# Kernel optimization log

Measured on AMD Instinct MI355X. Metric: run time of the kernel, lower is better.

## Reference

```python
import jax, jax.numpy as jnp
import numpy as np

DIM = 1024
HEADS = 16
HEAD_DIM = DIM // HEADS
FF = 4 * DIM


def setup_inputs() -> dict:
    key = jax.random.key(0)
    ks = jax.random.split(key, 16)
    s = 0.02
    return {
        "x": jax.random.normal(ks[0], (2, 2048, DIM), dtype=jnp.float32),
        "wq": jax.random.normal(ks[1], (DIM, DIM), dtype=jnp.float32) * s,
        "bq": jnp.zeros((DIM,), jnp.float32),
        "wk": jax.random.normal(ks[2], (DIM, DIM), dtype=jnp.float32) * s,
        "bk": jnp.zeros((DIM,), jnp.float32),
        "wv": jax.random.normal(ks[3], (DIM, DIM), dtype=jnp.float32) * s,
        "bv": jnp.zeros((DIM,), jnp.float32),
        "wo": jax.random.normal(ks[4], (DIM, DIM), dtype=jnp.float32) * s,
        "bo": jnp.zeros((DIM,), jnp.float32),
        "w1": jax.random.normal(ks[5], (DIM, FF), dtype=jnp.float32) * s,
        "b1": jnp.zeros((FF,), jnp.float32),
        "w2": jax.random.normal(ks[6], (FF, DIM), dtype=jnp.float32) * s,
        "b2": jnp.zeros((DIM,), jnp.float32),
        "g1": jnp.ones((DIM,), jnp.float32),
        "be1": jnp.zeros((DIM,), jnp.float32),
        "g2": jnp.ones((DIM,), jnp.float32),
        "be2": jnp.zeros((DIM,), jnp.float32),
    }


def _layernorm(x, g, b, eps=1e-5):
    mu = jnp.mean(x, axis=-1, keepdims=True)
    var = jnp.mean(jnp.square(x - mu), axis=-1, keepdims=True)
    return (x - mu) * jax.lax.rsqrt(var + eps) * g + b


def reference(x, wq, bq, wk, bk, wv, bv, wo, bo, w1, b1, w2, b2, g1, be1, g2, be2):
    B, T, D = x.shape
    normed = _layernorm(x, g1, be1)
    # [B,T,D] -> [B,H,T,hd]
    def heads(y):
        return y.reshape(B, T, HEADS, HEAD_DIM).transpose(0, 2, 1, 3)
    q = heads(normed @ wq + bq)
    k = heads(normed @ wk + bk)
    v = heads(normed @ wv + bv)
    scale = 1.0 / np.sqrt(HEAD_DIM).astype(np.float32)
    attn = jax.nn.softmax(jnp.einsum('bhqd,bhkd->bhqk', q, k) * scale, axis=-1)
    out = jnp.einsum('bhqk,bhkd->bhqd', attn, v)
    out = out.transpose(0, 2, 1, 3).reshape(B, T, D)
    x = x + out @ wo + bo
    h = _layernorm(x, g2, be2)
    ffn = jax.nn.gelu(h @ w1 + b1, approximate=False) @ w2 + b2
    return x + ffn
```

## Files before the change

kernel.cpp:

```cpp
#include <hip/hip_runtime.h>
#include <math.h>

#define DIM   1024
#define HEADS 16
#define HDIM  64
#define FFDIM 4096
#define MROWS 4096
#define SEQ   2048
#define QKVS  3072
#define SCALE_Q 0.1803368801111204f

typedef _Float16 f16x8 __attribute__((ext_vector_type(8)));
typedef _Float16 f16x4 __attribute__((ext_vector_type(4)));
typedef float    f32x4 __attribute__((ext_vector_type(4)));

#define GLOAD_LDS16(g, l) __builtin_amdgcn_global_load_lds(                 \
    (const __attribute__((address_space(1))) void*)(g),                     \
    (__attribute__((address_space(3))) void*)(l), 16, 0, 0)

__device__ __forceinline__ float gelu_exact(float x) {
    return 0.5f * x * (1.0f + erff(x * 0.70710678118654752f));
}

__device__ __forceinline__ int pk2(float a, float b) {
    union { _Float16 h[2]; int i; } u;
    u.h[0] = (_Float16)a; u.h[1] = (_Float16)b;
    return u.i;
}

__global__ __launch_bounds__(256) void ln_kernel(
    const float* __restrict__ x, const float* __restrict__ g,
    const float* __restrict__ b, _Float16* __restrict__ out)
{
    const int row = blockIdx.x;
    const int t   = threadIdx.x;
    const float4* xr = reinterpret_cast<const float4*>(x + (size_t)row * DIM);
    float4 v = xr[t];
    float s  = v.x + v.y + v.z + v.w;
    float ss = v.x*v.x + v.y*v.y + v.z*v.z + v.w*v.w;
    #pragma unroll
    for (int off = 32; off; off >>= 1) {
        s  += __shfl_down(s,  off);
        ss += __shfl_down(ss, off);
    }
    __shared__ float red[8];
    const int wave = t >> 6, lane = t & 63;
    if (lane == 0) { red[wave] = s; red[4 + wave] = ss; }
    __syncthreads();
    if (t == 0) {
        float S  = red[0] + red[1] + red[2] + red[3];
        float SS = red[4] + red[5] + red[6] + red[7];
        float mu  = S * (1.0f / DIM);
        float var = SS * (1.0f / DIM) - mu * mu;
        red[0] = mu;
        red[1] = rsqrtf(var + 1e-5f);
    }
    __syncthreads();
    const float mu = red[0], inv = red[1];
    const float4 gv = reinterpret_cast<const float4*>(g)[t];
    const float4 bv = reinterpret_cast<const float4*>(b)[t];
    f16x4 o;
    o[0] = (_Float16)((v.x - mu) * inv * gv.x + bv.x);
    o[1] = (_Float16)((v.y - mu) * inv * gv.y + bv.y);
    o[2] = (_Float16)((v.z - mu) * inv * gv.z + bv.z);
    o[3] = (_Float16)((v.w - mu) * inv * gv.w + bv.w);
    *reinterpret_cast<f16x4*>(out + (size_t)row * DIM + t * 4) = o;
}

__global__ void concat3(const float* __restrict__ a, const float* __restrict__ b,
                        const float* __restrict__ c, float* __restrict__ dst)
{
    const int i = blockIdx.x * 256 + threadIdx.x;
    if (i < 1024)      dst[i] = a[i];
    else if (i < 2048) dst[i] = b[i - 1024];
    else               dst[i] = c[i - 2048];
}

__global__ __launch_bounds__(256) void transpose_cvt(
    const float* __restrict__ src, _Float16* __restrict__ dst,
    int R, int C, int dstOff)
{
    __shared__ float t[32][33];
    const int c0 = blockIdx.x * 32, r0 = blockIdx.y * 32;
    const int tx = threadIdx.x & 31, ty = (threadIdx.x >> 5) * 4;
    #pragma unroll
    for (int i = 0; i < 4; ++i)
        t[ty + i][tx] = src[(size_t)(r0 + ty + i) * C + c0 + tx];
    __syncthreads();
    #pragma unroll
    for (int i = 0; i < 4; ++i)
        dst[(size_t)(dstOff + c0 + ty + i) * R + r0 + tx] = (_Float16)t[tx][ty + i];
}

template<int EPI>
__global__ __launch_bounds__(256) void gemm_mfma(
    const _Float16* __restrict__ A,
    const _Float16* __restrict__ Bt,
    const float* __restrict__ bias,
    const float* __restrict__ res,
    float* __restrict__ Cf,
    _Float16* __restrict__ Ch,
    _Float16* __restrict__ Qh, _Float16* __restrict__ Kh,
    _Float16* __restrict__ Vtp,
    int M, int N, int K)
{
    __shared__ __attribute__((aligned(16))) _Float16 As[128 * 32];
    __shared__ __attribute__((aligned(16))) _Float16 Bs[128 * 32];

    const int tid  = threadIdx.x;
    const int wave = tid >> 6;
    const int lane = tid & 63;
    const int bm = blockIdx.y * 128;
    const int bn = blockIdx.x * 128;
    const int wr = wave >> 1, wc = wave & 1;

    const int c0   = wave * 2;
    const int srow = lane >> 2;
    const int skc  = lane & 3;
    const _Float16* Ag = A  + (size_t)(bm + c0 * 16 + srow) * K + skc * 8;
    const _Float16* Bg = Bt + (size_t)(bn + c0 * 16 + srow) * K + skc * 8;
    _Float16* Al = As + c0 * 512;
    _Float16* Bl = Bs + c0 * 512;

    f32x4 acc[4][4] = {};

    const int fr = lane & 15;
    const int fk = (lane >> 4) * 8;

    for (int k0 = 0; k0 < K; k0 += 32) {
        __syncthreads();
        GLOAD_LDS16(Ag + k0,                  Al);
        GLOAD_LDS16(Ag + k0 + 16 * (size_t)K, Al + 512);
        GLOAD_LDS16(Bg + k0,                  Bl);
        GLOAD_LDS16(Bg + k0 + 16 * (size_t)K, Bl + 512);
        __syncthreads();

        f16x8 af[4], bfr[4];
        #pragma unroll
        for (int m = 0; m < 4; ++m)
            af[m] = *reinterpret_cast<const f16x8*>(As + (wr * 64 + m * 16 + fr) * 32 + fk);
        #pragma unroll
        for (int n = 0; n < 4; ++n)
            bfr[n] = *reinterpret_cast<const f16x8*>(Bs + (wc * 64 + n * 16 + fr) * 32 + fk);
        #pragma unroll
        for (int m = 0; m < 4; ++m)
            #pragma unroll
            for (int n = 0; n < 4; ++n)
                acc[m][n] = __builtin_amdgcn_mfma_f32_16x16x32_f16(
                    af[m], bfr[n], acc[m][n], 0, 0, 0);
    }

    const int fg = lane >> 4;
    #pragma unroll
    for (int m = 0; m < 4; ++m) {
        const int row0 = bm + wr * 64 + m * 16 + fg * 4;
        #pragma unroll
        for (int n = 0; n < 4; ++n) {
            const int col = bn + wc * 64 + n * 16 + fr;
            const float bv = bias[col];
            if constexpr (EPI == 3) {
                const int b  = row0 >> 11;
                const int t0 = row0 & 2047;
                const int sect = col >> 10;
                const int h = (col >> 6) & 15;
                const int d = col & 63;
                const size_t bh = (size_t)(b * 16 + h);
                if (sect == 0) {
                    #pragma unroll
                    for (int j = 0; j < 4; ++j)
                        Qh[(bh * 2048 + t0 + j) * 64 + d] =
                            (_Float16)((acc[m][n][j] + bv) * SCALE_Q);
                } else if (sect == 1) {
                    #pragma unroll
                    for (int j = 0; j < 4; ++j)
                        Kh[(bh * 2048 + t0 + j) * 64 + d] =
                            (_Float16)(acc[m][n][j] + bv);
                } else {
                    f16x4 pv;
                    #pragma unroll
                    for (int j = 0; j < 4; ++j)
                        pv[j] = (_Float16)(acc[m][n][j] + bv);
                    *reinterpret_cast<f16x4*>(Vtp + (bh * 64 + d) * 2048 + t0) = pv;
                }
            } else {
                #pragma unroll
                for (int j = 0; j < 4; ++j) {
                    const size_t idx = (size_t)(row0 + j) * N + col;
                    float v = acc[m][n][j] + bv;
                    if constexpr (EPI == 2) {
                        Ch[idx] = (_Float16)gelu_exact(v);
                    } else {
                        v += res[idx];
                        Cf[idx] = v;
                    }
                }
            }
        }
    }
}

__global__ __launch_bounds__(256) void attn_mfma(
    const _Float16* __restrict__ Qh, const _Float16* __restrict__ Kh,
    const _Float16* __restrict__ Vt, _Float16* __restrict__ O)
{
    __shared__ __attribute__((aligned(16))) _Float16 Kbuf[2][4096];
    __shared__ __attribute__((aligned(16))) _Float16 Vbuf[2][4096];

    const int fid = blockIdx.x;
    const int qt  = (fid >> 3) & 31;
    const int bh  = (fid & 7) * 4 + (fid >> 8);

    const int tid  = threadIdx.x;
    const int w    = tid >> 6;
    const int lane = tid & 63;
    const int fr   = lane & 15;
    const int g    = lane >> 4;

    const int srow_lo = lane >> 3;
    const int sc      = (lane & 7) ^ (srow_lo & 7);
    const int rowA = w * 8 + srow_lo;
    const int rowB = (w + 4) * 8 + srow_lo;
    const char* Kg = (const char*)(Kh + (size_t)bh * (2048 * 64));
    const char* Vg = (const char*)(Vt + (size_t)bh * (64 * 2048));

#define STAGE(nb, kt) do {                                                   \
    GLOAD_LDS16(Kg + ((size_t)(((kt) * 64 + rowA)) << 7) + (sc << 4),        \
                &Kbuf[nb][w * 512]);                                         \
    GLOAD_LDS16(Kg + ((size_t)(((kt) * 64 + rowB)) << 7) + (sc << 4),        \
                &Kbuf[nb][(w + 4) * 512]);                                   \
    GLOAD_LDS16(Vg + ((size_t)rowA << 12) + ((kt) << 7) + (sc << 4),         \
                &Vbuf[nb][w * 512]);                                         \
    GLOAD_LDS16(Vg + ((size_t)rowB << 12) + ((kt) << 7) + (sc << 4),         \
                &Vbuf[nb][(w + 4) * 512]);                                   \
} while (0)

    const int qrow = qt * 64 + w * 16 + fr;
    const f16x8* Qp = reinterpret_cast<const f16x8*>(
        Qh + ((size_t)bh * 2048 + qrow) * 64);
    const f16x8 qf0 = Qp[g];
    const f16x8 qf1 = Qp[4 + g];

    const int fr7 = fr & 7;
    const int cs0 = ((g ^ fr7) << 4);
    const int cs1 = (((4 + g) ^ fr7) << 4);

    f32x4 o[4] = {};
    float mrun = -INFINITY, l = 0.0f;

    const int idx0 = (fr + ((g & 1) << 5)) << 2;
    const int idx1 = idx0 + 64;
    const bool ghi = (g >= 2);

    STAGE(0, 0);
    __syncthreads();
    int cur = 0;

    for (int kt = 0; kt < 32; ++kt) {
        if (kt < 31) STAGE(cur ^ 1, kt + 1);

        f32x4 sT[4] = {};
        {
            const char* Kb = (const char*)Kbuf[cur];
            #pragma unroll
            for (int mm = 0; mm < 4; ++mm) {
                const char* rb = Kb + ((mm * 16 + fr) << 7);
                f16x8 ka = *reinterpret_cast<const f16x8*>(rb + cs0);
                f16x8 kb = *reinterpret_cast<const f16x8*>(rb + cs1);
                sT[mm] = __builtin_amdgcn_mfma_f32_16x16x32_f16(ka, qf0, sT[mm], 0, 0, 0);
                sT[mm] = __builtin_amdgcn_mfma_f32_16x16x32_f16(kb, qf1, sT[mm], 0, 0, 0);
            }
        }

        float pm = sT[0][0];
        #pragma unroll
        for (int mm = 0; mm < 4; ++mm)
            #pragma unroll
            for (int j = 0; j < 4; ++j) pm = fmaxf(pm, sT[mm][j]);
        pm = fmaxf(pm, __shfl_xor(pm, 16));
        pm = fmaxf(pm, __shfl_xor(pm, 32));
        const float mnew  = fmaxf(mrun, pm);
        const float alpha = exp2f(mrun - mnew);
        mrun = mnew;
        float rs = 0.0f;
        #pragma unroll
        for (int mm = 0; mm < 4; ++mm)
            #pragma unroll
            for (int j = 0; j < 4; ++j) {
                const float p = exp2f(sT[mm][j] - mnew);
                sT[mm][j] = p;
                rs += p;
            }
        rs += __shfl_xor(rs, 16);
        rs += __shfl_xor(rs, 32);
        l = l * alpha + rs;
        #pragma unroll
        for (int mm = 0; mm < 4; ++mm)
            #pragma unroll
            for (int j = 0; j < 4; ++j) o[mm][j] *= alpha;

        int pk[4][2];
        #pragma unroll
        for (int mm = 0; mm < 4; ++mm) {
            pk[mm][0] = pk2(sT[mm][0], sT[mm][1]);
            pk[mm][1] = pk2(sT[mm][2], sT[mm][3]);
        }

        union BF { int i[4]; f16x8 h; } bf0, bf1;
        #pragma unroll
        for (int s = 0; s < 2; ++s) {
            union BF* bf = s ? &bf1 : &bf0;
            const int rA = 2 * s, rB = 2 * s + 1;
            int a0 = __builtin_amdgcn_ds_bpermute(idx0, pk[rA][0]);
            int b0 = __builtin_amdgcn_ds_bpermute(idx0, pk[rB][0]);
            int a1 = __builtin_amdgcn_ds_bpermute(idx0, pk[rA][1]);
            int b1 = __builtin_amdgcn_ds_bpermute(idx0, pk[rB][1]);
            int a2 = __builtin_amdgcn_ds_bpermute(idx1, pk[rA][0]);
            int b2 = __builtin_amdgcn_ds_bpermute(idx1, pk[rB][0]);
            int a3 = __builtin_amdgcn_ds_bpermute(idx1, pk[rA][1]);
            int b3 = __builtin_amdgcn_ds_bpermute(idx1, pk[rB][1]);
            bf->i[0] = ghi ? b0 : a0;
            bf->i[1] = ghi ? b1 : a1;
            bf->i[2] = ghi ? b2 : a2;
            bf->i[3] = ghi ? b3 : a3;
        }

        {
            const char* Vb = (const char*)Vbuf[cur];
            #pragma unroll
            for (int mm = 0; mm < 4; ++mm) {
                const char* rb = Vb + ((mm * 16 + fr) << 7);
                f16x8 va = *reinterpret_cast<const f16x8*>(rb + cs0);
                f16x8 vb = *reinterpret_cast<const f16x8*>(rb + cs1);
                o[mm] = __builtin_amdgcn_mfma_f32_16x16x32_f16(va, bf0.h, o[mm], 0, 0, 0);
                o[mm] = __builtin_amdgcn_mfma_f32_16x16x32_f16(vb, bf1.h, o[mm], 0, 0, 0);
            }
        }

        __syncthreads();
        cur ^= 1;
    }
#undef STAGE

    const float linv = 1.0f / l;
    const int b = bh >> 4, h = bh & 15;
    _Float16* Op = O + (size_t)(b * 2048 + qt * 64 + w * 16 + fr) * DIM
                     + h * 64 + 4 * g;
    #pragma unroll
    for (int mm = 0; mm < 4; ++mm) {
        f16x4 st;
        #pragma unroll
        for (int j = 0; j < 4; ++j) st[j] = (_Float16)(o[mm][j] * linv);
        *reinterpret_cast<f16x4*>(Op + mm * 16) = st;
    }
}

extern "C" void kernel_launch(void* const* d_in, const int* in_sizes, int n_in,
                              void* d_out, int out_size, void* d_ws, size_t ws_size,
                              hipStream_t stream)
{
    const float* x   = (const float*)d_in[0];
    const float* wq  = (const float*)d_in[1];
    const float* bq  = (const float*)d_in[2];
    const float* wk  = (const float*)d_in[3];
    const float* bk  = (const float*)d_in[4];
    const float* wv  = (const float*)d_in[5];
    const float* bv  = (const float*)d_in[6];
    const float* wo  = (const float*)d_in[7];
    const float* bo  = (const float*)d_in[8];
    const float* w1  = (const float*)d_in[9];
    const float* b1  = (const float*)d_in[10];
    const float* w2  = (const float*)d_in[11];
    const float* b2  = (const float*)d_in[12];
    const float* g1  = (const float*)d_in[13];
    const float* be1 = (const float*)d_in[14];
    const float* g2  = (const float*)d_in[15];
    const float* be2 = (const float*)d_in[16];
    float* out = (float*)d_out;

    char* wsb = (char*)d_ws;
    _Float16* Wt     = (_Float16*)(wsb);
    _Float16* normed = (_Float16*)(wsb + ((size_t)8  << 20));
    _Float16* Qh     = (_Float16*)(wsb + ((size_t)16 << 20));
    _Float16* Kh     = (_Float16*)(wsb + ((size_t)24 << 20));
    _Float16* Vt     = (_Float16*)(wsb + ((size_t)32 << 20));
    _Float16* mid    = (_Float16*)(wsb + ((size_t)16 << 20));
    _Float16* attno  = (_Float16*)(wsb + ((size_t)40 << 20));
    float*    bqkv   = (float*)   (wsb + ((size_t)48 << 20));

    ln_kernel<<<MROWS, 256, 0, stream>>>(x, g1, be1, normed);
    concat3<<<12, 256, 0, stream>>>(bq, bk, bv, bqkv);
    transpose_cvt<<<dim3(32, 32), 256, 0, stream>>>(wq, Wt, 1024, 1024, 0);
    transpose_cvt<<<dim3(32, 32), 256, 0, stream>>>(wk, Wt, 1024, 1024, 1024);
    transpose_cvt<<<dim3(32, 32), 256, 0, stream>>>(wv, Wt, 1024, 1024, 2048);
    gemm_mfma<3><<<dim3(QKVS / 128, MROWS / 128), 256, 0, stream>>>(
        normed, Wt, bqkv, nullptr, nullptr, nullptr, Qh, Kh, Vt,
        MROWS, QKVS, DIM);
    attn_mfma<<<1024, 256, 0, stream>>>(Qh, Kh, Vt, attno);
    transpose_cvt<<<dim3(32, 32), 256, 0, stream>>>(wo, Wt, 1024, 1024, 0);
    gemm_mfma<1><<<dim3(DIM / 128, MROWS / 128), 256, 0, stream>>>(
        attno, Wt, bo, x, out, nullptr, nullptr, nullptr, nullptr,
        MROWS, DIM, DIM);
    ln_kernel<<<MROWS, 256, 0, stream>>>(out, g2, be2, normed);
    transpose_cvt<<<dim3(128, 32), 256, 0, stream>>>(w1, Wt, 1024, 4096, 0);
    gemm_mfma<2><<<dim3(FFDIM / 128, MROWS / 128), 256, 0, stream>>>(
        normed, Wt, b1, nullptr, nullptr, mid, nullptr, nullptr, nullptr,
        MROWS, FFDIM, DIM);
    transpose_cvt<<<dim3(32, 128), 256, 0, stream>>>(w2, Wt, 4096, 1024, 0);
    gemm_mfma<1><<<dim3(DIM / 128, MROWS / 128), 256, 0, stream>>>(
        mid, Wt, b2, out, out, nullptr, nullptr, nullptr, nullptr,
        MROWS, DIM, FFDIM);
}
```

Baseline: 475.6 us.

## Stage GEMM epilogues through LDS, shrink N=1024 GEMM tiles, lazy softmax rescale

```diff
diff --git a/kernel.cpp b/kernel.cpp
--- a/kernel.cpp
+++ b/kernel.cpp
@@ -92,7 +92,25 @@
         dst[(size_t)(dstOff + c0 + ty + i) * R + r0 + tx] = (_Float16)t[tx][ty + i];
 }
 
-template<int EPI>
+__global__ __launch_bounds__(256) void transpose_cvt3(
+    const float* __restrict__ s0, const float* __restrict__ s1,
+    const float* __restrict__ s2, _Float16* __restrict__ dst)
+{
+    __shared__ float t[32][33];
+    const float* src = blockIdx.z == 0 ? s0 : (blockIdx.z == 1 ? s1 : s2);
+    const int dstOff = blockIdx.z * 1024;
+    const int c0 = blockIdx.x * 32, r0 = blockIdx.y * 32;
+    const int tx = threadIdx.x & 31, ty = (threadIdx.x >> 5) * 4;
+    #pragma unroll
+    for (int i = 0; i < 4; ++i)
+        t[ty + i][tx] = src[(size_t)(r0 + ty + i) * 1024 + c0 + tx];
+    __syncthreads();
+    #pragma unroll
+    for (int i = 0; i < 4; ++i)
+        dst[(size_t)(dstOff + c0 + ty + i) * 1024 + r0 + tx] = (_Float16)t[tx][ty + i];
+}
+
+template<int EPI, int BM>
 __global__ __launch_bounds__(256) void gemm_mfma(
     const _Float16* __restrict__ A,
     const _Float16* __restrict__ Bt,
@@ -104,46 +122,49 @@
     _Float16* __restrict__ Vtp,
     int M, int N, int K)
 {
-    __shared__ __attribute__((aligned(16))) _Float16 As[128 * 32];
-    __shared__ __attribute__((aligned(16))) _Float16 Bs[128 * 32];
+    constexpr int MF  = BM / 32;
+    constexpr int ACH = BM / 64;
+    __shared__ __attribute__((aligned(16))) _Float16 SMEM[8192];
+    _Float16* As = SMEM;
+    _Float16* Bs = SMEM + BM * 32;
 
     const int tid  = threadIdx.x;
     const int wave = tid >> 6;
     const int lane = tid & 63;
-    const int bm = blockIdx.y * 128;
+    const int bm = blockIdx.y * BM;
     const int bn = blockIdx.x * 128;
     const int wr = wave >> 1, wc = wave & 1;
 
-    const int c0   = wave * 2;
     const int srow = lane >> 2;
     const int skc  = lane & 3;
-    const _Float16* Ag = A  + (size_t)(bm + c0 * 16 + srow) * K + skc * 8;
-    const _Float16* Bg = Bt + (size_t)(bn + c0 * 16 + srow) * K + skc * 8;
-    _Float16* Al = As + c0 * 512;
-    _Float16* Bl = Bs + c0 * 512;
-
-    f32x4 acc[4][4] = {};
+    const _Float16* Ag = A  + (size_t)(bm + wave * ACH * 16 + srow) * K + skc * 8;
+    const _Float16* Bg = Bt + (size_t)(bn + wave * 32 + srow) * K + skc * 8;
+    _Float16* Al = As + wave * ACH * 512;
+    _Float16* Bl = Bs + wave * 1024;
+
+    f32x4 acc[MF][4] = {};
 
     const int fr = lane & 15;
     const int fk = (lane >> 4) * 8;
 
     for (int k0 = 0; k0 < K; k0 += 32) {
         __syncthreads();
-        GLOAD_LDS16(Ag + k0,                  Al);
-        GLOAD_LDS16(Ag + k0 + 16 * (size_t)K, Al + 512);
+        #pragma unroll
+        for (int c = 0; c < ACH; ++c)
+            GLOAD_LDS16(Ag + k0 + (size_t)c * 16 * K, Al + c * 512);
         GLOAD_LDS16(Bg + k0,                  Bl);
         GLOAD_LDS16(Bg + k0 + 16 * (size_t)K, Bl + 512);
         __syncthreads();
 
-        f16x8 af[4], bfr[4];
-        #pragma unroll
-        for (int m = 0; m < 4; ++m)
-            af[m] = *reinterpret_cast<const f16x8*>(As + (wr * 64 + m * 16 + fr) * 32 + fk);
+        f16x8 af[MF], bfr[4];
+        #pragma unroll
+        for (int m = 0; m < MF; ++m)
+            af[m] = *reinterpret_cast<const f16x8*>(As + (wr * (BM/2) + m * 16 + fr) * 32 + fk);
         #pragma unroll
         for (int n = 0; n < 4; ++n)
             bfr[n] = *reinterpret_cast<const f16x8*>(Bs + (wc * 64 + n * 16 + fr) * 32 + fk);
         #pragma unroll
-        for (int m = 0; m < 4; ++m)
+        for (int m = 0; m < MF; ++m)
             #pragma unroll
             for (int n = 0; n < 4; ++n)
                 acc[m][n] = __builtin_amdgcn_mfma_f32_16x16x32_f16(
@@ -151,48 +172,92 @@
     }
 
     const int fg = lane >> 4;
-    #pragma unroll
-    for (int m = 0; m < 4; ++m) {
-        const int row0 = bm + wr * 64 + m * 16 + fg * 4;
-        #pragma unroll
-        for (int n = 0; n < 4; ++n) {
-            const int col = bn + wc * 64 + n * 16 + fr;
-            const float bv = bias[col];
-            if constexpr (EPI == 3) {
-                const int b  = row0 >> 11;
-                const int t0 = row0 & 2047;
-                const int sect = col >> 10;
-                const int h = (col >> 6) & 15;
-                const int d = col & 63;
-                const size_t bh = (size_t)(b * 16 + h);
-                if (sect == 0) {
-                    #pragma unroll
-                    for (int j = 0; j < 4; ++j)
-                        Qh[(bh * 2048 + t0 + j) * 64 + d] =
-                            (_Float16)((acc[m][n][j] + bv) * SCALE_Q);
-                } else if (sect == 1) {
-                    #pragma unroll
-                    for (int j = 0; j < 4; ++j)
-                        Kh[(bh * 2048 + t0 + j) * 64 + d] =
-                            (_Float16)(acc[m][n][j] + bv);
-                } else {
-                    f16x4 pv;
-                    #pragma unroll
-                    for (int j = 0; j < 4; ++j)
-                        pv[j] = (_Float16)(acc[m][n][j] + bv);
-                    *reinterpret_cast<f16x4*>(Vtp + (bh * 64 + d) * 2048 + t0) = pv;
-                }
-            } else {
+
+    if constexpr (EPI == 1) {
+        #pragma unroll
+        for (int m = 0; m < MF; ++m) {
+            const int row0 = bm + wr * (BM/2) + m * 16 + fg * 4;
+            #pragma unroll
+            for (int n = 0; n < 4; ++n) {
+                const int col = bn + wc * 64 + n * 16 + fr;
+                const float bv = bias[col];
                 #pragma unroll
                 for (int j = 0; j < 4; ++j) {
                     const size_t idx = (size_t)(row0 + j) * N + col;
-                    float v = acc[m][n][j] + bv;
-                    if constexpr (EPI == 2) {
-                        Ch[idx] = (_Float16)gelu_exact(v);
-                    } else {
-                        v += res[idx];
-                        Cf[idx] = v;
+                    Cf[idx] = acc[m][n][j] + bv + res[idx];
+                }
+            }
+        }
+        return;
+    }
+
+    _Float16* wtile = SMEM + wave * 2048;
+
+    const int sect = bn >> 10;
+    const int bidx = bm >> 11;
+    const int t0w  = (bm & 2047) + wr * (BM / 2);
+    const int hh   = ((bn & 1023) >> 6) + wc;
+    const size_t bh = (size_t)(bidx * 16 + hh);
+
+    #pragma unroll
+    for (int pass = 0; pass < MF / 2; ++pass) {
+        __syncthreads();
+        #pragma unroll
+        for (int mi = 0; mi < 2; ++mi) {
+            const int mm = pass * 2 + mi;
+            #pragma unroll
+            for (int n = 0; n < 4; ++n) {
+                const int cl = n * 16 + fr;
+                const float bv = bias[bn + wc * 64 + cl];
+                #pragma unroll
+                for (int j = 0; j < 4; ++j) {
+                    const int rl = mi * 16 + fg * 4 + j;
+                    float v = acc[mm][n][j] + bv;
+                    _Float16 hv;
+                    if constexpr (EPI == 2) hv = (_Float16)gelu_exact(v);
+                    else hv = (_Float16)(sect == 0 ? v * SCALE_Q : v);
+                    wtile[rl * 64 + ((((cl >> 3) ^ (rl & 7))) << 3) + (cl & 7)] = hv;
+                }
+            }
+        }
+        __syncthreads();
+
+        if constexpr (EPI == 2) {
+            _Float16* dst = Ch + (size_t)(bm + wr * (BM/2) + pass * 32) * N
+                               + bn + wc * 64;
+            #pragma unroll
+            for (int it = 0; it < 4; ++it) {
+                const int rl = it * 8 + (lane >> 3);
+                const int ch = lane & 7;
+                f16x8 vv = *reinterpret_cast<const f16x8*>(
+                    wtile + rl * 64 + ((ch ^ (rl & 7)) << 3));
+                *reinterpret_cast<f16x8*>(dst + (size_t)rl * N + ch * 8) = vv;
+            }
+        } else {
+            if (sect < 2) {
+                _Float16* dst = (sect == 0 ? Qh : Kh)
+                              + (bh * 2048 + t0w + pass * 32) * 64;
+                #pragma unroll
+                for (int it = 0; it < 4; ++it) {
+                    const int rl = it * 8 + (lane >> 3);
+                    const int ch = lane & 7;
+                    f16x8 vv = *reinterpret_cast<const f16x8*>(
+                        wtile + rl * 64 + ((ch ^ (rl & 7)) << 3));
+                    *reinterpret_cast<f16x8*>(dst + (size_t)rl * 64 + ch * 8) = vv;
+                }
+            } else {
+                _Float16* dst = Vtp + bh * (64 * 2048) + t0w + pass * 32;
+                #pragma unroll
+                for (int it = 0; it < 4; ++it) {
+                    const int d   = it * 16 + (lane >> 2);
+                    const int tch = lane & 3;
+                    f16x8 vv;
+                    #pragma unroll
+                    for (int u = 0; u < 8; ++u) {
+                        const int rl = tch * 8 + u;
+                        vv[u] = wtile[rl * 64 + (((d >> 3) ^ (rl & 7)) << 3) + (d & 7)];
                     }
+                    *reinterpret_cast<f16x8*>(dst + (size_t)d * 2048 + tch * 8) = vv;
                 }
             }
         }
@@ -278,25 +343,28 @@
             for (int j = 0; j < 4; ++j) pm = fmaxf(pm, sT[mm][j]);
         pm = fmaxf(pm, __shfl_xor(pm, 16));
         pm = fmaxf(pm, __shfl_xor(pm, 32));
-        const float mnew  = fmaxf(mrun, pm);
-        const float alpha = exp2f(mrun - mnew);
-        mrun = mnew;
+        if (!__all(pm - mrun <= 8.0f)) {
+            const float mnew  = fmaxf(mrun, pm);
+            const float alpha = exp2f(mrun - mnew);
+            mrun = mnew;
+            l *= alpha;
+            #pragma unroll
+            for (int mm = 0; mm < 4; ++mm)
+                #pragma unroll
+                for (int j = 0; j < 4; ++j) o[mm][j] *= alpha;
+        }
         float rs = 0.0f;
         #pragma unroll
         for (int mm = 0; mm < 4; ++mm)
             #pragma unroll
             for (int j = 0; j < 4; ++j) {
-                const float p = exp2f(sT[mm][j] - mnew);
+                const float p = exp2f(sT[mm][j] - mrun);
                 sT[mm][j] = p;
                 rs += p;
             }
         rs += __shfl_xor(rs, 16);
         rs += __shfl_xor(rs, 32);
-        l = l * alpha + rs;
-        #pragma unroll
-        for (int mm = 0; mm < 4; ++mm)
-            #pragma unroll
-            for (int j = 0; j < 4; ++j) o[mm][j] *= alpha;
+        l += rs;
 
         int pk[4][2];
         #pragma unroll
@@ -389,24 +457,22 @@
 
     ln_kernel<<<MROWS, 256, 0, stream>>>(x, g1, be1, normed);
     concat3<<<12, 256, 0, stream>>>(bq, bk, bv, bqkv);
-    transpose_cvt<<<dim3(32, 32), 256, 0, stream>>>(wq, Wt, 1024, 1024, 0);
-    transpose_cvt<<<dim3(32, 32), 256, 0, stream>>>(wk, Wt, 1024, 1024, 1024);
-    transpose_cvt<<<dim3(32, 32), 256, 0, stream>>>(wv, Wt, 1024, 1024, 2048);
-    gemm_mfma<3><<<dim3(QKVS / 128, MROWS / 128), 256, 0, stream>>>(
+    transpose_cvt3<<<dim3(32, 32, 3), 256, 0, stream>>>(wq, wk, wv, Wt);
+    gemm_mfma<3, 128><<<dim3(QKVS / 128, MROWS / 128), 256, 0, stream>>>(
         normed, Wt, bqkv, nullptr, nullptr, nullptr, Qh, Kh, Vt,
         MROWS, QKVS, DIM);
     attn_mfma<<<1024, 256, 0, stream>>>(Qh, Kh, Vt, attno);
     transpose_cvt<<<dim3(32, 32), 256, 0, stream>>>(wo, Wt, 1024, 1024, 0);
-    gemm_mfma<1><<<dim3(DIM / 128, MROWS / 128), 256, 0, stream>>>(
+    gemm_mfma<1, 64><<<dim3(DIM / 128, MROWS / 64), 256, 0, stream>>>(
         attno, Wt, bo, x, out, nullptr, nullptr, nullptr, nullptr,
         MROWS, DIM, DIM);
     ln_kernel<<<MROWS, 256, 0, stream>>>(out, g2, be2, normed);
     transpose_cvt<<<dim3(128, 32), 256, 0, stream>>>(w1, Wt, 1024, 4096, 0);
-    gemm_mfma<2><<<dim3(FFDIM / 128, MROWS / 128), 256, 0, stream>>>(
+    gemm_mfma<2, 128><<<dim3(FFDIM / 128, MROWS / 128), 256, 0, stream>>>(
         normed, Wt, b1, nullptr, nullptr, mid, nullptr, nullptr, nullptr,
         MROWS, FFDIM, DIM);
     transpose_cvt<<<dim3(32, 128), 256, 0, stream>>>(w2, Wt, 4096, 1024, 0);
-    gemm_mfma<1><<<dim3(DIM / 128, MROWS / 128), 256, 0, stream>>>(
+    gemm_mfma<1, 64><<<dim3(DIM / 128, MROWS / 64), 256, 0, stream>>>(
         mid, Wt, b2, out, out, nullptr, nullptr, nullptr, nullptr,
         MROWS, DIM, FFDIM);
 }
```

Result: faster. 457.3 us (-3.8%).
